# Performance work log

Measured on AMD Instinct MI355X. Metric: run time of the kernel, lower is better.

## Reference

```python
import jax, jax.numpy as jnp
import numpy as np

N_EMBED = 1024
HEAD_SIZE = 128

def setup_inputs() -> dict:
    key = jax.random.key(0)
    kx, kq, kk, kv = jax.random.split(key, 4)
    B, T = 8, 2048
    x = jax.random.normal(kx, (B, T, N_EMBED), dtype=jnp.float32)
    s = 1.0 / np.sqrt(N_EMBED)
    Wq = jax.random.normal(kq, (N_EMBED, HEAD_SIZE), dtype=jnp.float32) * s
    Wk = jax.random.normal(kk, (N_EMBED, HEAD_SIZE), dtype=jnp.float32) * s
    Wv = jax.random.normal(kv, (N_EMBED, HEAD_SIZE), dtype=jnp.float32) * s
    return {"x": x, "Wq": Wq, "Wk": Wk, "Wv": Wv}

def reference(x, Wq, Wk, Wv):
    # x: [B, T, E]; single-head causal attention (nanoGPT-style Head)
    B, T, E = x.shape
    q = jnp.einsum('bte,eh->bth', x, Wq)  # [B,T,H]
    k = jnp.einsum('bte,eh->bth', x, Wk)
    v = jnp.einsum('bte,eh->bth', x, Wv)
    scale = 1.0 / jnp.sqrt(jnp.asarray(q.shape[-1], dtype=x.dtype))
    wei = jnp.einsum('bqh,bkh->bqk', q, k) * scale  # [B,T,T]
    causal = jnp.tril(jnp.ones((T, T), dtype=bool))
    wei = jnp.where(causal[None, :, :], wei, jnp.asarray(-jnp.inf, dtype=wei.dtype))
    attn = jax.nn.softmax(wei, axis=-1)
    out = jnp.einsum('bqk,bkh->bqh', attn, v)  # [B,T,H]
    return out
```

## Files before the change

kernel.cpp:

```cpp
#include <hip/hip_runtime.h>
#include <hip/hip_bf16.h>

typedef __bf16 bf16_t;
typedef bf16_t bf16x8 __attribute__((ext_vector_type(8)));
typedef bf16_t bf16x4 __attribute__((ext_vector_type(4)));
typedef float f32x4 __attribute__((ext_vector_type(4)));

#define MFMA16(a, b, c) __builtin_amdgcn_mfma_f32_16x16x32_bf16((a), (b), (c), 0, 0, 0)

#define TT 2048
#define EE 1024
#define HH 128
#define UPB 288


__global__ __launch_bounds__(256) void prep_w_kernel(
    const float* __restrict__ Wq, const float* __restrict__ Wk,
    const float* __restrict__ Wv, bf16_t* __restrict__ Wt)
{
    int idx = blockIdx.x * 256 + threadIdx.x;
    int w = idx >> 17;
    int r = idx & 131071;
    int n = r >> 10, k = r & 1023;
    const float* W = (w == 0) ? Wq : (w == 1) ? Wk : Wv;
    Wt[idx] = (bf16_t)W[k * HH + n];
}

__global__ __launch_bounds__(256) void qkv_kernel(
    const float* __restrict__ x, const bf16_t* __restrict__ Wt,
    bf16_t* __restrict__ Qf, bf16_t* __restrict__ Kf, bf16_t* __restrict__ Vf)
{
    __shared__ __attribute__((aligned(16))) bf16_t As[2][64][40];
    const int row0 = blockIdx.x * 64;
    const int tid  = threadIdx.x;
    const int lane = tid & 63;
    const int wn   = tid >> 6;
    const int g = lane >> 4, c = lane & 15;

    const int row_a = tid >> 3;
    const int row_b = 32 + row_a;
    const int col4  = (tid & 7) * 4;
    const float* xA = x + (size_t)(row0 + row_a) * EE + col4;
    const float* xB = x + (size_t)(row0 + row_b) * EE + col4;

    const bf16_t* wrow[6];
    for (int nt = 0; nt < 6; ++nt) {
        int cb = wn * 96 + nt * 16;
        wrow[nt] = Wt + ((size_t)(cb >> 7) * HH + (cb & 127) + c) * EE + g * 8;
    }

    f32x4 acc[4][6];
    for (int i = 0; i < 4; ++i)
        for (int j = 0; j < 6; ++j) acc[i][j] = (f32x4)0.0f;

    float4 f0, f1;
#define STAGE_LOAD(T) do {                                                    \
    f0 = *reinterpret_cast<const float4*>(xA + (size_t)(T) * 32);             \
    f1 = *reinterpret_cast<const float4*>(xB + (size_t)(T) * 32);             \
} while (0)
#define STAGE_WRITE(BUF) do {                                                 \
    union { bf16_t h[4]; unsigned long long u; } p0, p1;                      \
    p0.h[0] = (bf16_t)f0.x; p0.h[1] = (bf16_t)f0.y;                           \
    p0.h[2] = (bf16_t)f0.z; p0.h[3] = (bf16_t)f0.w;                           \
    p1.h[0] = (bf16_t)f1.x; p1.h[1] = (bf16_t)f1.y;                           \
    p1.h[2] = (bf16_t)f1.z; p1.h[3] = (bf16_t)f1.w;                           \
    *reinterpret_cast<unsigned long long*>(&As[BUF][row_a][col4]) = p0.u;     \
    *reinterpret_cast<unsigned long long*>(&As[BUF][row_b][col4]) = p1.u;     \
} while (0)
#define COMPUTE(BUF, WREG) do {                                               \
    for (int mt = 0; mt < 4; ++mt) {                                          \
        bf16x8 af = *reinterpret_cast<const bf16x8*>(&As[BUF][mt * 16 + c][g * 8]); \
        for (int nt = 0; nt < 6; ++nt)                                        \
            acc[mt][nt] = MFMA16(af, WREG[nt], acc[mt][nt]);                  \
    } } while (0)

    bf16x8 wA[6], wB[6];
    for (int nt = 0; nt < 6; ++nt) wA[nt] = *(const bf16x8*)(wrow[nt]);
    STAGE_LOAD(0);
    STAGE_WRITE(0);
    __syncthreads();

    for (int t = 0; t < 32; t += 2) {
        if (t + 1 < 32) {
            STAGE_LOAD(t + 1);
            for (int nt = 0; nt < 6; ++nt)
                wB[nt] = *(const bf16x8*)(wrow[nt] + (size_t)(t + 1) * 32);
        }
        COMPUTE(0, wA);
        if (t + 1 < 32) STAGE_WRITE(1);
        __syncthreads();
        if (t + 1 >= 32) break;

        if (t + 2 < 32) {
            STAGE_LOAD(t + 2);
            for (int nt = 0; nt < 6; ++nt)
                wA[nt] = *(const bf16x8*)(wrow[nt] + (size_t)(t + 2) * 32);
        }
        COMPUTE(1, wB);
        if (t + 2 < 32) STAGE_WRITE(0);
        __syncthreads();
    }
#undef STAGE_LOAD
#undef STAGE_WRITE
#undef COMPUTE

    const float sc = 0.08838834764831845f * 1.4426950408889634f;
    for (int mt = 0; mt < 4; ++mt)
        for (int nt = 0; nt < 6; ++nt) {
            int cb = wn * 96 + nt * 16;
            int w  = cb >> 7;
            int hl = (cb & 127) + c;
            int t0 = row0 + mt * 16 + g * 4;
            if (w == 2) {
                int b  = t0 >> 11;
                int t  = t0 & (TT - 1);
                int vc = t >> 5, gg = (t & 31) >> 3, j0 = t & 7;
                int hb = hl >> 4, cc = hl & 15;
                union { bf16_t h4[4]; unsigned long long u; } pk;
                for (int i = 0; i < 4; ++i) pk.h4[i] = (bf16_t)acc[mt][nt][i];
                *reinterpret_cast<unsigned long long*>(
                    Vf + ((size_t)((b * 64 + vc) * 8 + hb)) * 512 +
                    (gg * 16 + cc) * 8 + j0) = pk.u;
            } else {
                bf16_t* dst = (w == 0) ? Qf : Kf;
                float s = (w == 0) ? sc : 1.0f;
                int kk = hl >> 5, gg = (hl & 31) >> 3, e = hl & 7;
                int grt = t0 >> 4;
                for (int i = 0; i < 4; ++i) {
                    int cr = (t0 + i) & 15;
                    dst[((size_t)(grt * 4 + kk)) * 512 + (gg * 16 + cr) * 8 + e] =
                        (bf16_t)(acc[mt][nt][i] * s);
                }
            }
        }
}

__global__ __launch_bounds__(256) void attn_kernel(
    const bf16_t* __restrict__ Qf, const bf16_t* __restrict__ Kf,
    const bf16_t* __restrict__ Vf, bf16_t* __restrict__ Pacc,
    float* __restrict__ Pml)
{
    __shared__ __attribute__((aligned(16))) bf16_t Pl[4][32][40];
    const int tid = threadIdx.x, lane = tid & 63, wid = tid >> 6;
    const int g = lane >> 4, c = lane & 15;
    bf16_t (*P)[40] = Pl[wid];

    const int bx = blockIdx.x;
    const int b  = bx & 7;
    const int u  = 287 - ((bx >> 3) * 4 + wid);
    int k = 0;
    while (4 * (k + 1) * (k + 2) <= u) ++k;
    const int r  = u - 4 * k * (k + 1);
    const int qt = 8 * k + r / (k + 1);
    const int ch = r - (r / (k + 1)) * (k + 1);
    const int q0 = qt * 32;
    const int kv_lo = ch * 256;
    int kv_hi = kv_lo + 256; if (kv_hi > q0 + 32) kv_hi = q0 + 32;
    const int sid = b * UPB + 4 * k * (k + 1) + (qt & 7) * (k + 1) + ch;

    bf16x8 qA[4], qB[4];
    for (int kk = 0; kk < 4; ++kk) {
        qA[kk] = *(const bf16x8*)(Qf +
            ((size_t)((b * 128 + (q0 >> 4)) * 4 + kk)) * 512 + lane * 8);
        qB[kk] = *(const bf16x8*)(Qf +
            ((size_t)((b * 128 + (q0 >> 4) + 1) * 4 + kk)) * 512 + lane * 8);
    }

    f32x4 accA[8], accB[8];
    for (int hb = 0; hb < 8; ++hb) { accA[hb] = (f32x4)0.0f; accB[hb] = (f32x4)0.0f; }
    float lsA[4] = {0, 0, 0, 0}, lsB[4] = {0, 0, 0, 0};

    for (int kv0 = kv_lo; kv0 < kv_hi; kv0 += 32) {
        const int kt = b * 128 + (kv0 >> 4);
        bf16x8 k0f[4], k1f[4], vf[8];
        for (int kk = 0; kk < 4; ++kk) {
            k0f[kk] = *(const bf16x8*)(Kf + ((size_t)(kt * 4 + kk)) * 512 + lane * 8);
            k1f[kk] = *(const bf16x8*)(Kf + ((size_t)((kt + 1) * 4 + kk)) * 512 + lane * 8);
        }
        const int vcb = (b * 64 + (kv0 >> 5)) * 8;
        for (int hb = 0; hb < 8; ++hb)
            vf[hb] = *(const bf16x8*)(Vf + ((size_t)(vcb + hb)) * 512 + lane * 8);

        f32x4 sA0 = (f32x4)0.0f, sA1 = (f32x4)0.0f;
        f32x4 sB0 = (f32x4)0.0f, sB1 = (f32x4)0.0f;
        for (int kk = 0; kk < 4; ++kk) {
            sA0 = MFMA16(qA[kk], k0f[kk], sA0);
            sA1 = MFMA16(qA[kk], k1f[kk], sA1);
            sB0 = MFMA16(qB[kk], k0f[kk], sB0);
            sB1 = MFMA16(qB[kk], k1f[kk], sB1);
        }
        if (kv0 + 32 > q0) {
            for (int i = 0; i < 4; ++i) {
                int row = q0 + g * 4 + i;
                if (kv0 + c > row)      sA0[i] = -1e30f;
                if (kv0 + 16 + c > row) sA1[i] = -1e30f;
            }
        }
        if (kv0 + 32 > q0 + 16) {
            for (int i = 0; i < 4; ++i) {
                int row = q0 + 16 + g * 4 + i;
                if (kv0 + c > row)      sB0[i] = -1e30f;
                if (kv0 + 16 + c > row) sB1[i] = -1e30f;
            }
        }
        float pA0[4], pA1[4], pB0[4], pB1[4];
        for (int i = 0; i < 4; ++i) {
            pA0[i] = exp2f(sA0[i]); pA1[i] = exp2f(sA1[i]);
            pB0[i] = exp2f(sB0[i]); pB1[i] = exp2f(sB1[i]);
            lsA[i] += pA0[i] + pA1[i];
            lsB[i] += pB0[i] + pB1[i];
        }
        for (int i = 0; i < 4; ++i) {
            P[g * 4 + i][c]           = (bf16_t)pA0[i];
            P[g * 4 + i][c + 16]      = (bf16_t)pA1[i];
            P[16 + g * 4 + i][c]      = (bf16_t)pB0[i];
            P[16 + g * 4 + i][c + 16] = (bf16_t)pB1[i];
        }
        __builtin_amdgcn_wave_barrier();
        asm volatile("s_waitcnt lgkmcnt(0)" ::: "memory");
        __builtin_amdgcn_sched_barrier(0);
        bf16x8 paA = *(const bf16x8*)&P[c][g * 8];
        bf16x8 paB = *(const bf16x8*)&P[16 + c][g * 8];
        __builtin_amdgcn_s_setprio(1);
        for (int hb = 0; hb < 8; ++hb) {
            accA[hb] = MFMA16(paA, vf[hb], accA[hb]);
            accB[hb] = MFMA16(paB, vf[hb], accB[hb]);
        }
        __builtin_amdgcn_s_setprio(0);
        __builtin_amdgcn_wave_barrier();
    }

    for (int off = 1; off < 16; off <<= 1)
        for (int i = 0; i < 4; ++i) {
            lsA[i] += __shfl_xor(lsA[i], off, 64);
            lsB[i] += __shfl_xor(lsB[i], off, 64);
        }
    if (c == 0)
        for (int i = 0; i < 4; ++i) {
            Pml[(size_t)sid * 32 + g * 4 + i]      = lsA[i];
            Pml[(size_t)sid * 32 + 16 + g * 4 + i] = lsB[i];
        }

    bf16_t* po = Pacc + (size_t)sid * (32 * 128);
    for (int hb = 0; hb < 8; ++hb) {
        union { bf16_t h4[4]; unsigned long long u; } pa, pb;
        for (int i = 0; i < 4; ++i) {
            pa.h4[i] = (bf16_t)accA[hb][i];
            pb.h4[i] = (bf16_t)accB[hb][i];
        }
        bf16_t* cp = po + (hb * 16 + c) * 32;
        *reinterpret_cast<unsigned long long*>(cp + g * 4)      = pa.u;
        *reinterpret_cast<unsigned long long*>(cp + 16 + g * 4) = pb.u;
    }
}

__global__ __launch_bounds__(128) void combine_kernel(
    const bf16_t* __restrict__ Pacc, const float* __restrict__ Pml,
    float* __restrict__ out)
{
    __shared__ float invL[32];
    const int qt = blockIdx.x;
    const int b  = blockIdx.y;
    const int k  = qt >> 3;
    const int base  = b * UPB + 4 * k * (k + 1) + (qt & 7) * (k + 1);
    const int count = k + 1;
    const int tid = threadIdx.x;

    if (tid < 32) {
        float L = 0.0f;
        for (int cu = 0; cu < count; ++cu)
            L += Pml[(size_t)(base + cu) * 32 + tid];
        invL[tid] = 1.0f / L;
    }
    __syncthreads();

    float s[32];
    for (int r = 0; r < 32; ++r) s[r] = 0.0f;
    for (int cu = 0; cu < count; ++cu) {
        const bf16_t* cp = Pacc + (size_t)(base + cu) * 4096 + tid * 32;
        for (int r8 = 0; r8 < 4; ++r8) {
            bf16x8 v = *(const bf16x8*)(cp + r8 * 8);
            for (int j = 0; j < 8; ++j) s[r8 * 8 + j] += (float)v[j];
        }
    }
    const int q0 = qt * 32;
    for (int r = 0; r < 32; ++r)
        out[((size_t)b * TT + q0 + r) * HH + tid] = s[r] * invL[r];
}

extern "C" void kernel_launch(void* const* d_in, const int* in_sizes, int n_in,
                              void* d_out, int out_size, void* d_ws, size_t ws_size,
                              hipStream_t stream)
{
    const float* x  = (const float*)d_in[0];
    const float* Wq = (const float*)d_in[1];
    const float* Wk = (const float*)d_in[2];
    const float* Wv = (const float*)d_in[3];

    char* ws = (char*)d_ws;
    bf16_t* Wt   = (bf16_t*)ws;
    bf16_t* Qf   = (bf16_t*)(ws + (1u  << 20));
    bf16_t* Kf   = (bf16_t*)(ws + (5u  << 20));
    bf16_t* Vf   = (bf16_t*)(ws + (9u  << 20));
    bf16_t* Pacc = (bf16_t*)(ws + (13u << 20));
    float*  Pml  = (float*) (ws + (32u << 20));

    prep_w_kernel<<<1536, 256, 0, stream>>>(Wq, Wk, Wv, Wt);
    qkv_kernel<<<256, 256, 0, stream>>>(x, Wt, Qf, Kf, Vf);
    attn_kernel<<<576, 256, 0, stream>>>(Qf, Kf, Vf, Pacc, Pml);
    combine_kernel<<<dim3(64, 8), 128, 0, stream>>>(Pacc, Pml, (float*)d_out);
}
```

Baseline: 80.79 us.

## Halve QKV projection row tile and deepen global-load prefetch pipeline

The QKV projection kernel now handles 32 rows per block instead of 64 and launches 512 blocks instead of 256, so more of the device's compute units get work. The x loads are prefetched three stages ahead in a rotating register buffer, and weight fragments are loaded two stages ahead. The K loop is fully unrolled. In exchange, each weight fragment is reused across fewer rows, so total weight traffic from L2 doubles.

```diff
diff --git a/kernel.cpp b/kernel.cpp
--- a/kernel.cpp
+++ b/kernel.cpp
@@ -30,18 +30,16 @@
     const float* __restrict__ x, const bf16_t* __restrict__ Wt,
     bf16_t* __restrict__ Qf, bf16_t* __restrict__ Kf, bf16_t* __restrict__ Vf)
 {
-    __shared__ __attribute__((aligned(16))) bf16_t As[2][64][40];
-    const int row0 = blockIdx.x * 64;
+    __shared__ __attribute__((aligned(16))) bf16_t As[2][32][40];
+    const int row0 = blockIdx.x * 32;
     const int tid  = threadIdx.x;
     const int lane = tid & 63;
     const int wn   = tid >> 6;
     const int g = lane >> 4, c = lane & 15;
-
-    const int row_a = tid >> 3;
-    const int row_b = 32 + row_a;
-    const int col4  = (tid & 7) * 4;
-    const float* xA = x + (size_t)(row0 + row_a) * EE + col4;
-    const float* xB = x + (size_t)(row0 + row_b) * EE + col4;
+    const int srow = tid >> 3;
+    const int scol = (tid & 7) * 4;
+
+    const float* xp = x + (size_t)(row0 + srow) * EE + scol;
 
     const bf16_t* wrow[6];
     for (int nt = 0; nt < 6; ++nt) {
@@ -49,72 +47,55 @@
         wrow[nt] = Wt + ((size_t)(cb >> 7) * HH + (cb & 127) + c) * EE + g * 8;
     }
 
-    f32x4 acc[4][6];
-    for (int i = 0; i < 4; ++i)
+    f32x4 acc[2][6];
+    for (int i = 0; i < 2; ++i)
         for (int j = 0; j < 6; ++j) acc[i][j] = (f32x4)0.0f;
 
-    float4 f0, f1;
-#define STAGE_LOAD(T) do {                                                    \
-    f0 = *reinterpret_cast<const float4*>(xA + (size_t)(T) * 32);             \
-    f1 = *reinterpret_cast<const float4*>(xB + (size_t)(T) * 32);             \
+    f32x4 pf[3];
+    bf16x8 w[2][6];
+
+#define WRITEPF(S, BUF) do {                                                  \
+    union { bf16_t h[4]; unsigned long long u; } pk_;                         \
+    pk_.h[0] = (bf16_t)pf[S][0]; pk_.h[1] = (bf16_t)pf[S][1];                 \
+    pk_.h[2] = (bf16_t)pf[S][2]; pk_.h[3] = (bf16_t)pf[S][3];                 \
+    *reinterpret_cast<unsigned long long*>(&As[BUF][srow][scol]) = pk_.u;     \
 } while (0)
-#define STAGE_WRITE(BUF) do {                                                 \
-    union { bf16_t h[4]; unsigned long long u; } p0, p1;                      \
-    p0.h[0] = (bf16_t)f0.x; p0.h[1] = (bf16_t)f0.y;                           \
-    p0.h[2] = (bf16_t)f0.z; p0.h[3] = (bf16_t)f0.w;                           \
-    p1.h[0] = (bf16_t)f1.x; p1.h[1] = (bf16_t)f1.y;                           \
-    p1.h[2] = (bf16_t)f1.z; p1.h[3] = (bf16_t)f1.w;                           \
-    *reinterpret_cast<unsigned long long*>(&As[BUF][row_a][col4]) = p0.u;     \
-    *reinterpret_cast<unsigned long long*>(&As[BUF][row_b][col4]) = p1.u;     \
-} while (0)
-#define COMPUTE(BUF, WREG) do {                                               \
-    for (int mt = 0; mt < 4; ++mt) {                                          \
-        bf16x8 af = *reinterpret_cast<const bf16x8*>(&As[BUF][mt * 16 + c][g * 8]); \
-        for (int nt = 0; nt < 6; ++nt)                                        \
-            acc[mt][nt] = MFMA16(af, WREG[nt], acc[mt][nt]);                  \
-    } } while (0)
-
-    bf16x8 wA[6], wB[6];
-    for (int nt = 0; nt < 6; ++nt) wA[nt] = *(const bf16x8*)(wrow[nt]);
-    STAGE_LOAD(0);
-    STAGE_WRITE(0);
+
+    pf[0] = *(const f32x4*)(xp);
+    pf[1] = *(const f32x4*)(xp + 32);
+    pf[2] = *(const f32x4*)(xp + 64);
+    for (int nt = 0; nt < 6; ++nt) w[0][nt] = *(const bf16x8*)(wrow[nt]);
+    for (int nt = 0; nt < 6; ++nt) w[1][nt] = *(const bf16x8*)(wrow[nt] + 32);
+    WRITEPF(0, 0);
     __syncthreads();
 
-    for (int t = 0; t < 32; t += 2) {
-        if (t + 1 < 32) {
-            STAGE_LOAD(t + 1);
+#pragma unroll
+    for (int t = 0; t < 32; ++t) {
+        if (t + 3 < 32) pf[(t + 3) % 3] = *(const f32x4*)(xp + (size_t)(t + 3) * 32);
+        for (int mt = 0; mt < 2; ++mt) {
+            bf16x8 af = *(const bf16x8*)&As[t & 1][mt * 16 + c][g * 8];
             for (int nt = 0; nt < 6; ++nt)
-                wB[nt] = *(const bf16x8*)(wrow[nt] + (size_t)(t + 1) * 32);
-        }
-        COMPUTE(0, wA);
-        if (t + 1 < 32) STAGE_WRITE(1);
+                acc[mt][nt] = MFMA16(af, w[t & 1][nt], acc[mt][nt]);
+        }
+        if (t + 2 < 32)
+            for (int nt = 0; nt < 6; ++nt)
+                w[t & 1][nt] = *(const bf16x8*)(wrow[nt] + (size_t)(t + 2) * 32);
+        if (t + 1 < 32) WRITEPF((t + 1) % 3, (t + 1) & 1);
         __syncthreads();
-        if (t + 1 >= 32) break;
-
-        if (t + 2 < 32) {
-            STAGE_LOAD(t + 2);
-            for (int nt = 0; nt < 6; ++nt)
-                wA[nt] = *(const bf16x8*)(wrow[nt] + (size_t)(t + 2) * 32);
-        }
-        COMPUTE(1, wB);
-        if (t + 2 < 32) STAGE_WRITE(0);
-        __syncthreads();
-    }
-#undef STAGE_LOAD
-#undef STAGE_WRITE
-#undef COMPUTE
+    }
+#undef WRITEPF
 
     const float sc = 0.08838834764831845f * 1.4426950408889634f;
-    for (int mt = 0; mt < 4; ++mt)
+    for (int mt = 0; mt < 2; ++mt)
         for (int nt = 0; nt < 6; ++nt) {
             int cb = wn * 96 + nt * 16;
-            int w  = cb >> 7;
+            int w_  = cb >> 7;
             int hl = (cb & 127) + c;
             int t0 = row0 + mt * 16 + g * 4;
-            if (w == 2) {
+            if (w_ == 2) {
                 int b  = t0 >> 11;
-                int t  = t0 & (TT - 1);
-                int vc = t >> 5, gg = (t & 31) >> 3, j0 = t & 7;
+                int tt = t0 & (TT - 1);
+                int vc = tt >> 5, gg = (tt & 31) >> 3, j0 = tt & 7;
                 int hb = hl >> 4, cc = hl & 15;
                 union { bf16_t h4[4]; unsigned long long u; } pk;
                 for (int i = 0; i < 4; ++i) pk.h4[i] = (bf16_t)acc[mt][nt][i];
@@ -122,8 +103,8 @@
                     Vf + ((size_t)((b * 64 + vc) * 8 + hb)) * 512 +
                     (gg * 16 + cc) * 8 + j0) = pk.u;
             } else {
-                bf16_t* dst = (w == 0) ? Qf : Kf;
-                float s = (w == 0) ? sc : 1.0f;
+                bf16_t* dst = (w_ == 0) ? Qf : Kf;
+                float s = (w_ == 0) ? sc : 1.0f;
                 int kk = hl >> 5, gg = (hl & 31) >> 3, e = hl & 7;
                 int grt = t0 >> 4;
                 for (int i = 0; i < 4; ++i) {
@@ -306,7 +287,7 @@
     float*  Pml  = (float*) (ws + (32u << 20));
 
     prep_w_kernel<<<1536, 256, 0, stream>>>(Wq, Wk, Wv, Wt);
-    qkv_kernel<<<256, 256, 0, stream>>>(x, Wt, Qf, Kf, Vf);
+    qkv_kernel<<<512, 256, 0, stream>>>(x, Wt, Qf, Kf, Vf);
     attn_kernel<<<576, 256, 0, stream>>>(Qf, Kf, Vf, Pacc, Pml);
     combine_kernel<<<dim3(64, 8), 128, 0, stream>>>(Pacc, Pml, (float*)d_out);
 }
```

Measured after the change: 92.72 us. 1.15x slower.
